# Kernel optimization log

Measured on AMD Instinct MI355X. Metric: run time of the kernel, lower is better.

Reference implementation:

```python
import jax, jax.numpy as jnp
import numpy as np

D_EMB, D_ENC, D_DEC, NH = 128, 256, 512, 8
HD = D_DEC // NH  # 64
LN_EPS = 1e-5


def lstm_scan(x_seq, h0, c0, W_ih, W_hh, b):
    # x_seq: [L, B, D_in]; PyTorch gate order i, f, g, o
    def step(carry, x_t):
        h, c = carry
        g = x_t @ W_ih.T + h @ W_hh.T + b
        i, f, gg, o = jnp.split(g, 4, axis=-1)
        c = jax.nn.sigmoid(f) * c + jax.nn.sigmoid(i) * jnp.tanh(gg)
        h = jax.nn.sigmoid(o) * jnp.tanh(c)
        return (h, c), h
    (h, c), hs = jax.lax.scan(step, (h0, c0), x_seq)
    return hs, h, c


def setup_inputs() -> dict:
    key = jax.random.key(0)
    ks = iter(jax.random.split(key, 32))
    B, L, V, NC, T = 64, 64, 32000, 2, 32
    s = 0.05
    nrm = lambda shape: jax.random.normal(next(ks), shape, jnp.float32) * s
    return dict(
        nx=jax.random.randint(next(ks), (B, L), 0, V),
        label=jax.random.randint(next(ks), (B,), 0, NC),
        start_emb=nrm((1, D_EMB)),
        tok_emb=nrm((V, D_EMB)),
        style_emb=nrm((NC, D_DEC)),
        enc_Wih_f=nrm((4 * D_ENC, D_EMB)), enc_Whh_f=nrm((4 * D_ENC, D_ENC)), enc_b_f=nrm((4 * D_ENC,)),
        enc_Wih_b=nrm((4 * D_ENC, D_EMB)), enc_Whh_b=nrm((4 * D_ENC, D_ENC)), enc_b_b=nrm((4 * D_ENC,)),
        transfer_W=nrm((D_DEC, 2 * D_ENC)),
        dec_Wih=nrm((4 * D_DEC, D_EMB)), dec_Whh=nrm((4 * D_DEC, D_DEC)), dec_b=nrm((4 * D_DEC,)),
        attn_in_w=nrm((3 * D_DEC, D_DEC)), attn_in_b=nrm((3 * D_DEC,)),
        attn_out_w=nrm((D_DEC, D_DEC)), attn_out_b=nrm((D_DEC,)),
        proj_W=nrm((V, D_DEC)), proj_b=nrm((V,)),
        ln_g=jnp.ones((D_DEC,), jnp.float32), ln_b=jnp.zeros((D_DEC,), jnp.float32),
        max_len=T,
    )


def reference(nx, label, start_emb, tok_emb, style_emb,
              enc_Wih_f, enc_Whh_f, enc_b_f, enc_Wih_b, enc_Whh_b, enc_b_b,
              transfer_W, dec_Wih, dec_Whh, dec_b,
              attn_in_w, attn_in_b, attn_out_w, attn_out_b,
              proj_W, proj_b, ln_g, ln_b, max_len):
    B, L = nx.shape
    x = tok_emb[nx]                      # [B, L, 128] (dropout = identity, eval)
    xs = jnp.transpose(x, (1, 0, 2))     # [L, B, 128]
    z = jnp.zeros((B, D_ENC), x.dtype)
    hs_f, hf, _ = lstm_scan(xs, z, z, enc_Wih_f, enc_Whh_f, enc_b_f)
    hs_b, hb, _ = lstm_scan(xs[::-1], z, z, enc_Wih_b, enc_Whh_b, enc_b_b)
    memory = jnp.concatenate([hs_f, hs_b[::-1]], axis=-1)        # [L, B, 512]
    h0 = jnp.tanh(jnp.concatenate([hf, hb], -1) @ transfer_W.T)  # [B, 512]
    c0 = style_emb[label]                                        # [B, 512]

    Wq, Wk, Wv = jnp.split(attn_in_w, 3, axis=0)
    bq, bk, bv = jnp.split(attn_in_b, 3, axis=0)
    k = (memory @ Wk.T + bk).reshape(L, B, NH, HD)
    v = (memory @ Wv.T + bv).reshape(L, B, NH, HD)
    scale = 1.0 / np.sqrt(HD).astype(np.float32)

    x0 = jnp.broadcast_to(start_emb[0], (B, D_EMB))

    def step(carry, _):
        h, c, xe = carry
        # LSTM cell (decoder, single step)
        g = xe @ dec_Wih.T + h @ dec_Whh.T + dec_b
        i, f, gg, o = jnp.split(g, 4, axis=-1)
        c = jax.nn.sigmoid(f) * c + jax.nn.sigmoid(i) * jnp.tanh(gg)
        h_ = jax.nn.sigmoid(o) * jnp.tanh(c)                     # [B, 512]
        # single-query multi-head attention against memory
        q = ((h_ @ Wq.T + bq) * scale).reshape(B, NH, HD)
        att = jax.nn.softmax(jnp.einsum('bhd,lbhd->bhl', q, k), axis=-1)
        ctx = jnp.einsum('bhl,lbhd->bhd', att, v).reshape(B, D_DEC)
        a = ctx @ attn_out_w.T + attn_out_b
        # residual + LayerNorm
        y = h_ + a
        mu = y.mean(-1, keepdims=True)
        var = ((y - mu) ** 2).mean(-1, keepdims=True)
        h = (y - mu) / jnp.sqrt(var + LN_EPS) * ln_g + ln_b
        logits_t = h @ proj_W.T + proj_b                         # [B, V]
        xe = tok_emb[jnp.argmax(logits_t, axis=-1)]              # greedy feedback
        return (h, c, xe), logits_t

    _, logits = jax.lax.scan(step, (h0, c0, x0), None, length=max_len)
    return jnp.transpose(logits, (1, 0, 2))  # [B, T, V]
```

## Files before the change

### kernel.cpp

```cpp
#include <hip/hip_runtime.h>
#include <hip/hip_bf16.h>
#include <math.h>

#define L_SEQ 64
#define B_SZ  64
#define DEMB  128
#define DENC  256
#define DDEC  512
#define NHD   8
#define HDIM  64
#define VSZ   32000
#define TDEC  32

typedef unsigned long long ull;

__device__ __forceinline__ float sigm(float x){ return 1.0f/(1.0f+expf(-x)); }
__device__ __forceinline__ int rfl(int x){ return __builtin_amdgcn_readfirstlane(x); }
__device__ __forceinline__ unsigned fmono(float f){
    unsigned u = __float_as_uint(f);
    return (u & 0x80000000u) ? ~u : (u | 0x80000000u);
}

__global__ void k_init(float* hTe, float* cTe, float* xeT, const float* start_emb){
    int i = blockIdx.x*256 + threadIdx.x;
    int stride = gridDim.x*256;
    for (int j = i; j < 2*2*DENC*B_SZ; j += stride) hTe[j] = 0.f;
    for (int j = i; j < 2*DENC*B_SZ;   j += stride) cTe[j] = 0.f;
    for (int j = i; j < DEMB*B_SZ;     j += stride) xeT[j] = start_emb[j >> 6];
}

__global__ void k_embed(const int* nx, const float* tok_emb, float* xT){
    int t = blockIdx.x;
    for (int j = threadIdx.x; j < B_SZ*DEMB; j += 256){
        int b = j >> 7; int k = j & 127;
        int row = nx[b*L_SEQ + t];
        xT[(t*DEMB + k)*B_SZ + b] = tok_emb[(size_t)row*DEMB + k];
    }
}

__global__ void k_pregates(const float* xT, const float* Wf, const float* bf,
                           const float* Wb, const float* bb, float* GpreT){
    int wid  = (blockIdx.x*256 + threadIdx.x) >> 6;
    int lane = threadIdx.x & 63;
    for (int job = wid; job < 2*L_SEQ*1024; job += 2048){
        int dir = rfl(job >> 16);
        int rem = job & 65535;
        int t   = rfl(rem >> 10);
        int row = rfl(rem & 1023);
        const float* W = dir ? Wb : Wf;
        float acc = (dir ? bb : bf)[row];
        const float4* W4 = (const float4*)(W + (size_t)row*DEMB);
        const float* xr = xT + (size_t)t*DEMB*B_SZ + lane;
        #pragma unroll 4
        for (int k4 = 0; k4 < DEMB/4; ++k4){
            float4 w = W4[k4];
            const float* hp = xr + k4*4*B_SZ;
            acc += w.x*hp[0] + w.y*hp[B_SZ] + w.z*hp[2*B_SZ] + w.w*hp[3*B_SZ];
        }
        GpreT[(size_t)job*B_SZ + lane] = acc;
    }
}

__global__ void k_enc_step(int s, const float* __restrict__ GpreT,
                           const float* __restrict__ Whh_f, const float* __restrict__ Whh_b,
                           float* hTe, float* cTe, float* memT){
    int wid  = blockIdx.x;
    int lane = threadIdx.x & 63;
    int dir = rfl(wid >> 8);
    int u   = rfl(wid & 255);
    int tpre = dir ? (63 - s) : s;
    const float* Gp = GpreT + (size_t)(dir*L_SEQ + tpre)*1024*B_SZ;
    float gi = Gp[(u      )*B_SZ + lane];
    float gf = Gp[(u + 256)*B_SZ + lane];
    float gg = Gp[(u + 512)*B_SZ + lane];
    float go = Gp[(u + 768)*B_SZ + lane];
    const float* hT  = hTe + (size_t)(s&1)*(2*DENC*B_SZ) + dir*DENC*B_SZ;
    float*       hTn = hTe + (size_t)((s+1)&1)*(2*DENC*B_SZ) + dir*DENC*B_SZ;
    const float* W = dir ? Whh_b : Whh_f;
    const float4* Wi = (const float4*)(W + (size_t)(u      )*DENC);
    const float4* Wf = (const float4*)(W + (size_t)(u + 256)*DENC);
    const float4* Wg = (const float4*)(W + (size_t)(u + 512)*DENC);
    const float4* Wo = (const float4*)(W + (size_t)(u + 768)*DENC);
    #pragma unroll 4
    for (int k4 = 0; k4 < DENC/4; ++k4){
        float4 wi = Wi[k4], wf = Wf[k4], wg = Wg[k4], wo = Wo[k4];
        const float* hp = hT + k4*4*B_SZ + lane;
        float h0 = hp[0], h1 = hp[B_SZ], h2 = hp[2*B_SZ], h3 = hp[3*B_SZ];
        gi += wi.x*h0 + wi.y*h1 + wi.z*h2 + wi.w*h3;
        gf += wf.x*h0 + wf.y*h1 + wf.z*h2 + wf.w*h3;
        gg += wg.x*h0 + wg.y*h1 + wg.z*h2 + wg.w*h3;
        go += wo.x*h0 + wo.y*h1 + wo.z*h2 + wo.w*h3;
    }
    float c  = cTe[(dir*DENC + u)*B_SZ + lane];
    float cn = sigm(gf)*c + sigm(gi)*tanhf(gg);
    float hn = sigm(go)*tanhf(cn);
    cTe[(dir*DENC + u)*B_SZ + lane] = cn;
    hTn[u*B_SZ + lane] = hn;
    int tmem = dir ? (63 - s) : s;
    memT[((size_t)tmem*DDEC + dir*DENC + u)*B_SZ + lane] = hn;
}

__global__ void k_h0(const float* hTe, const float* transfer_W, const float* style_emb,
                     const int* label, float* hTd, float* cTd){
    int u    = rfl((int)blockIdx.x);
    int lane = threadIdx.x & 63;
    const float* hf = hTe;
    const float* hb = hTe + DENC*B_SZ;
    float acc = 0.f;
    const float4* W4 = (const float4*)(transfer_W + (size_t)u*DDEC);
    #pragma unroll 4
    for (int k4 = 0; k4 < 64; ++k4){
        float4 w = W4[k4];
        const float* hp = hf + k4*4*B_SZ + lane;
        acc += w.x*hp[0] + w.y*hp[B_SZ] + w.z*hp[2*B_SZ] + w.w*hp[3*B_SZ];
    }
    #pragma unroll 4
    for (int k4 = 64; k4 < 128; ++k4){
        float4 w = W4[k4];
        const float* hp = hb + (k4-64)*4*B_SZ + lane;
        acc += w.x*hp[0] + w.y*hp[B_SZ] + w.z*hp[2*B_SZ] + w.w*hp[3*B_SZ];
    }
    hTd[u*B_SZ + lane] = tanhf(acc);
    cTd[u*B_SZ + lane] = style_emb[(size_t)label[lane]*DDEC + u];
}

__global__ void k_kv(const float* memT, const float* attn_in_w, const float* attn_in_b,
                     float* kT, float* vv){
    int wid  = (blockIdx.x*256 + threadIdx.x) >> 6;
    int lane = threadIdx.x & 63;
    for (int job = wid; job < L_SEQ*1024; job += 2048){
        int t   = rfl(job >> 10);
        int row = rfl(job & 1023);
        int wrow = 512 + row;
        const float4* W4 = (const float4*)(attn_in_w + (size_t)wrow*DDEC);
        float acc = attn_in_b[wrow];
        const float* mp = memT + (size_t)t*DDEC*B_SZ + lane;
        #pragma unroll 4
        for (int k4 = 0; k4 < 128; ++k4){
            float4 w = W4[k4];
            const float* hp = mp + k4*4*B_SZ;
            acc += w.x*hp[0] + w.y*hp[B_SZ] + w.z*hp[2*B_SZ] + w.w*hp[3*B_SZ];
        }
        if (row < 512){
            int h = row >> 6, d = row & 63;
            kT[(((size_t)lane*NHD + h)*HDIM + d)*L_SEQ + t] = acc;
        } else {
            int r2 = row - 512; int h = r2 >> 6, d = r2 & 63;
            vv[(((size_t)lane*NHD + h)*L_SEQ + t)*HDIM + d] = acc;
        }
    }
}

__global__ void k_gates(const float* __restrict__ xeT, const float* __restrict__ hTd, float* cTd,
                        const float* __restrict__ Wih, const float* __restrict__ Whh,
                        const float* __restrict__ bias, float* h_row){
    int u    = rfl((int)blockIdx.x);
    int lane = threadIdx.x & 63;
    float gi = bias[u], gf = bias[u+512], gg = bias[u+1024], go = bias[u+1536];
    {
        const float4* Wi = (const float4*)(Wih + (size_t)(u       )*DEMB);
        const float4* Wf = (const float4*)(Wih + (size_t)(u + 512 )*DEMB);
        const float4* Wg = (const float4*)(Wih + (size_t)(u + 1024)*DEMB);
        const float4* Wo = (const float4*)(Wih + (size_t)(u + 1536)*DEMB);
        #pragma unroll 4
        for (int k4 = 0; k4 < DEMB/4; ++k4){
            float4 wi = Wi[k4], wf = Wf[k4], wg = Wg[k4], wo = Wo[k4];
            const float* hp = xeT + k4*4*B_SZ + lane;
            float h0 = hp[0], h1 = hp[B_SZ], h2 = hp[2*B_SZ], h3 = hp[3*B_SZ];
            gi += wi.x*h0 + wi.y*h1 + wi.z*h2 + wi.w*h3;
            gf += wf.x*h0 + wf.y*h1 + wf.z*h2 + wf.w*h3;
            gg += wg.x*h0 + wg.y*h1 + wg.z*h2 + wg.w*h3;
            go += wo.x*h0 + wo.y*h1 + wo.z*h2 + wo.w*h3;
        }
    }
    {
        const float4* Wi = (const float4*)(Whh + (size_t)(u       )*DDEC);
        const float4* Wf = (const float4*)(Whh + (size_t)(u + 512 )*DDEC);
        const float4* Wg = (const float4*)(Whh + (size_t)(u + 1024)*DDEC);
        const float4* Wo = (const float4*)(Whh + (size_t)(u + 1536)*DDEC);
        #pragma unroll 4
        for (int k4 = 0; k4 < DDEC/4; ++k4){
            float4 wi = Wi[k4], wf = Wf[k4], wg = Wg[k4], wo = Wo[k4];
            const float* hp = hTd + k4*4*B_SZ + lane;
            float h0 = hp[0], h1 = hp[B_SZ], h2 = hp[2*B_SZ], h3 = hp[3*B_SZ];
            gi += wi.x*h0 + wi.y*h1 + wi.z*h2 + wi.w*h3;
            gf += wf.x*h0 + wf.y*h1 + wf.z*h2 + wf.w*h3;
            gg += wg.x*h0 + wg.y*h1 + wg.z*h2 + wg.w*h3;
            go += wo.x*h0 + wo.y*h1 + wo.z*h2 + wo.w*h3;
        }
    }
    float c  = cTd[u*B_SZ + lane];
    float cn = sigm(gf)*c + sigm(gi)*tanhf(gg);
    float h_ = sigm(go)*tanhf(cn);
    cTd[u*B_SZ + lane] = cn;
    h_row[(size_t)lane*DDEC + u] = h_;
}

__global__ void __launch_bounds__(256) k_attn(
        const float* __restrict__ h_row, const float* __restrict__ kT, const float* __restrict__ vv,
        const float* __restrict__ attn_in_w, const float* __restrict__ attn_in_b,
        const float* __restrict__ attn_out_w, const float* __restrict__ attn_out_b,
        const float* __restrict__ ln_g, const float* __restrict__ ln_b,
        float* hTd, float* hLN_row){
    int b = blockIdx.x, tid = threadIdx.x;
    __shared__ float hs[512], qs[512], ss[512], cx[512], ys[512];
    __shared__ float ssum[8];
    __shared__ float red[256];
    hs[tid]     = h_row[(size_t)b*512 + tid];
    hs[tid+256] = h_row[(size_t)b*512 + tid + 256];
    __syncthreads();
    for (int r = 0; r < 2; ++r){
        int row = tid + r*256;
        float acc = attn_in_b[row];
        const float4* W4 = (const float4*)(attn_in_w + (size_t)row*512);
        #pragma unroll 4
        for (int k4 = 0; k4 < 128; ++k4){
            float4 w = W4[k4];
            acc += w.x*hs[k4*4] + w.y*hs[k4*4+1] + w.z*hs[k4*4+2] + w.w*hs[k4*4+3];
        }
        qs[row] = acc * 0.125f;
    }
    __syncthreads();
    for (int r = 0; r < 2; ++r){
        int job = tid + r*256; int h = job >> 6, l = job & 63;
        const float* kp = kT + ((size_t)b*NHD + h)*HDIM*L_SEQ + l;
        float acc = 0.f;
        #pragma unroll 8
        for (int d = 0; d < 64; ++d) acc += qs[h*64 + d] * kp[d*64];
        ss[job] = acc;
    }
    __syncthreads();
    if (tid < 8){
        float m = -1e30f;
        for (int l = 0; l < 64; ++l) m = fmaxf(m, ss[tid*64 + l]);
        float s = 0.f;
        for (int l = 0; l < 64; ++l){ float e = expf(ss[tid*64 + l] - m); ss[tid*64 + l] = e; s += e; }
        ssum[tid] = s;
    }
    __syncthreads();
    for (int r = 0; r < 2; ++r){
        int job = tid + r*256; int h = job >> 6, d = job & 63;
        const float* vp = vv + ((size_t)b*NHD + h)*L_SEQ*HDIM + d;
        float acc = 0.f;
        #pragma unroll 8
        for (int l = 0; l < 64; ++l) acc += ss[h*64 + l] * vp[l*HDIM];
        cx[job] = acc / ssum[h];
    }
    __syncthreads();
    for (int r = 0; r < 2; ++r){
        int row = tid + r*256;
        float acc = attn_out_b[row];
        const float4* W4 = (const float4*)(attn_out_w + (size_t)row*512);
        #pragma unroll 4
        for (int k4 = 0; k4 < 128; ++k4){
            float4 w = W4[k4];
            acc += w.x*cx[k4*4] + w.y*cx[k4*4+1] + w.z*cx[k4*4+2] + w.w*cx[k4*4+3];
        }
        ys[row] = hs[row] + acc;
    }
    __syncthreads();
    red[tid] = ys[tid] + ys[tid+256];
    __syncthreads();
    for (int off = 128; off > 0; off >>= 1){ if (tid < off) red[tid] += red[tid+off]; __syncthreads(); }
    float mu = red[0] * (1.f/512.f);
    __syncthreads();
    float d0 = ys[tid] - mu, d1 = ys[tid+256] - mu;
    red[tid] = d0*d0 + d1*d1;
    __syncthreads();
    for (int off = 128; off > 0; off >>= 1){ if (tid < off) red[tid] += red[tid+off]; __syncthreads(); }
    float rstd = 1.f / sqrtf(red[0]*(1.f/512.f) + 1e-5f);
    for (int r = 0; r < 2; ++r){
        int i = tid + r*256;
        float hv = (ys[i] - mu) * rstd * ln_g[i] + ln_b[i];
        hLN_row[(size_t)b*512 + i] = hv;
        hTd[(size_t)i*64 + b] = hv;
    }
}

__global__ void __launch_bounds__(256) k_proj(int t, const float* __restrict__ hTd,
                       const float* __restrict__ proj_W, const float* __restrict__ proj_b,
                       float* __restrict__ out, ull* __restrict__ partials){
    int wid  = (blockIdx.x*256 + threadIdx.x) >> 6;
    int lane = threadIdx.x & 63;
    int n0 = rfl(wid << 4);
    float acc[16];
    #pragma unroll
    for (int j = 0; j < 16; ++j) acc[j] = proj_b[n0 + j];
    const float* W = proj_W + (size_t)n0*DDEC;
    #pragma unroll 2
    for (int k4 = 0; k4 < 128; ++k4){
        float h0 = hTd[(k4*4+0)*B_SZ + lane];
        float h1 = hTd[(k4*4+1)*B_SZ + lane];
        float h2 = hTd[(k4*4+2)*B_SZ + lane];
        float h3 = hTd[(k4*4+3)*B_SZ + lane];
        #pragma unroll
        for (int j = 0; j < 16; ++j){
            float4 w = *(const float4*)(W + (size_t)j*DDEC + k4*4);
            acc[j] += w.x*h0 + w.y*h1 + w.z*h2 + w.w*h3;
        }
    }
    ull m = 0;
    float* op = out + (size_t)lane*(TDEC*VSZ) + (size_t)t*VSZ + n0;
    #pragma unroll
    for (int j = 0; j < 16; ++j){
        op[j] = acc[j];
        ull p = ((ull)fmono(acc[j]) << 32) | (unsigned)(~(unsigned)(n0 + j));
        m = (p > m) ? p : m;
    }
    partials[(size_t)lane*2048 + wid] = m;
}

__global__ void k_fin(const ull* __restrict__ partials, const float* __restrict__ tok_emb, float* xeT){
    int b = blockIdx.x, tid = threadIdx.x;
    __shared__ ull red[128];
    __shared__ int sidx;
    ull m = 0;
    for (int j = tid; j < 2000; j += 128){
        ull p = partials[(size_t)b*2048 + j];
        if (p > m) m = p;
    }
    red[tid] = m; __syncthreads();
    for (int off = 64; off > 0; off >>= 1){
        if (tid < off){ if (red[tid+off] > red[tid]) red[tid] = red[tid+off]; }
        __syncthreads();
    }
    if (tid == 0) sidx = (int)(~(unsigned)(red[0] & 0xffffffffull));
    __syncthreads();
    int idx = sidx;
    xeT[tid*B_SZ + b] = tok_emb[(size_t)idx*DEMB + tid];
}

extern "C" void kernel_launch(void* const* d_in, const int* in_sizes, int n_in,
                              void* d_out, int out_size, void* d_ws, size_t ws_size,
                              hipStream_t stream){
    (void)in_sizes; (void)n_in; (void)out_size; (void)ws_size;
    const int*   nx        = (const int*)d_in[0];
    const int*   label     = (const int*)d_in[1];
    const float* start_emb = (const float*)d_in[2];
    const float* tok_emb   = (const float*)d_in[3];
    const float* style_emb = (const float*)d_in[4];
    const float* enc_Wih_f = (const float*)d_in[5];
    const float* enc_Whh_f = (const float*)d_in[6];
    const float* enc_b_f   = (const float*)d_in[7];
    const float* enc_Wih_b = (const float*)d_in[8];
    const float* enc_Whh_b = (const float*)d_in[9];
    const float* enc_b_b   = (const float*)d_in[10];
    const float* transfer_W= (const float*)d_in[11];
    const float* dec_Wih   = (const float*)d_in[12];
    const float* dec_Whh   = (const float*)d_in[13];
    const float* dec_b     = (const float*)d_in[14];
    const float* attn_in_w = (const float*)d_in[15];
    const float* attn_in_b = (const float*)d_in[16];
    const float* attn_out_w= (const float*)d_in[17];
    const float* attn_out_b= (const float*)d_in[18];
    const float* proj_W    = (const float*)d_in[19];
    const float* proj_b    = (const float*)d_in[20];
    const float* ln_g      = (const float*)d_in[21];
    const float* ln_b      = (const float*)d_in[22];
    float* out = (float*)d_out;
    float* ws  = (float*)d_ws;

    size_t off = 0;
    float* xT    = ws + off; off += (size_t)L_SEQ*DEMB*B_SZ;
    float* GpreT = ws + off; off += (size_t)2*L_SEQ*1024*B_SZ;
    float* memT  = ws + off; off += (size_t)L_SEQ*DDEC*B_SZ;
    float* kT    = ws + off; off += (size_t)B_SZ*NHD*HDIM*L_SEQ;
    float* vv    = ws + off; off += (size_t)B_SZ*NHD*L_SEQ*HDIM;
    float* hTe   = ws + off; off += 2*2*DENC*B_SZ;
    float* cTe   = ws + off; off += 2*DENC*B_SZ;
    float* hTd   = ws + off; off += DDEC*B_SZ;
    float* cTd   = ws + off; off += DDEC*B_SZ;
    float* h_row = ws + off; off += B_SZ*DDEC;
    float* hLN   = ws + off; off += B_SZ*DDEC;
    float* xeT   = ws + off; off += DEMB*B_SZ;
    ull* partials = (ull*)(ws + off); off += (size_t)B_SZ*2048*2;

    k_init<<<64, 256, 0, stream>>>(hTe, cTe, xeT, start_emb);
    k_embed<<<64, 256, 0, stream>>>(nx, tok_emb, xT);
    k_pregates<<<512, 256, 0, stream>>>(xT, enc_Wih_f, enc_b_f, enc_Wih_b, enc_b_b, GpreT);
    for (int s = 0; s < 64; ++s)
        k_enc_step<<<512, 64, 0, stream>>>(s, GpreT, enc_Whh_f, enc_Whh_b, hTe, cTe, memT);
    k_h0<<<512, 64, 0, stream>>>(hTe, transfer_W, style_emb, label, hTd, cTd);
    k_kv<<<512, 256, 0, stream>>>(memT, attn_in_w, attn_in_b, kT, vv);
    for (int t = 0; t < 32; ++t){
        k_gates<<<512, 64, 0, stream>>>(xeT, hTd, cTd, dec_Wih, dec_Whh, dec_b, h_row);
        k_attn<<<64, 256, 0, stream>>>(h_row, kT, vv, attn_in_w, attn_in_b,
                                       attn_out_w, attn_out_b, ln_g, ln_b, hTd, hLN);
        k_proj<<<500, 256, 0, stream>>>(t, hTd, proj_W, proj_b, out, partials);
        k_fin<<<64, 128, 0, stream>>>(partials, tok_emb, xeT);
    }
}
```

Before: 9.384 ms.

## Register-block pregates and K/V projections; reduce argmax partials per block

The encoder input-gate and attention K/V projection kernels now have each wavefront compute 16 output rows at once. Each activation load is reused across those 16 rows instead of being reloaded per row, with __restrict__ and launch bounds added. The projection kernel writes logits with float4 stores and does a block-level shared-memory max before writing partials. This cuts partials per batch row from 2000 to 500, so the final argmax kernel reads less. The cost is higher register pressure and fewer parallel jobs in the pregate and K/V kernels.

```diff
diff --git a/kernel.cpp b/kernel.cpp
--- a/kernel.cpp
+++ b/kernel.cpp
@@ -38,26 +38,34 @@
     }
 }
 
-__global__ void k_pregates(const float* xT, const float* Wf, const float* bf,
-                           const float* Wb, const float* bb, float* GpreT){
+__global__ void __launch_bounds__(256) k_pregates(
+        const float* __restrict__ xT, const float* __restrict__ Wf, const float* __restrict__ bf,
+        const float* __restrict__ Wb, const float* __restrict__ bb, float* __restrict__ GpreT){
     int wid  = (blockIdx.x*256 + threadIdx.x) >> 6;
     int lane = threadIdx.x & 63;
-    for (int job = wid; job < 2*L_SEQ*1024; job += 2048){
-        int dir = rfl(job >> 16);
-        int rem = job & 65535;
-        int t   = rfl(rem >> 10);
-        int row = rfl(rem & 1023);
-        const float* W = dir ? Wb : Wf;
-        float acc = (dir ? bb : bf)[row];
-        const float4* W4 = (const float4*)(W + (size_t)row*DEMB);
+    for (int job = wid; job < 2*L_SEQ*64; job += 2048){
+        int dir = rfl(job >> 12);
+        int rem = job & 4095;
+        int t   = rfl(rem >> 6);
+        int n0  = rfl((rem & 63) << 4);
+        const float* W = (dir ? Wb : Wf) + (size_t)n0*DEMB;
+        const float* bias = dir ? bb : bf;
+        float acc[16];
+        #pragma unroll
+        for (int j = 0; j < 16; ++j) acc[j] = bias[n0 + j];
         const float* xr = xT + (size_t)t*DEMB*B_SZ + lane;
-        #pragma unroll 4
         for (int k4 = 0; k4 < DEMB/4; ++k4){
-            float4 w = W4[k4];
-            const float* hp = xr + k4*4*B_SZ;
-            acc += w.x*hp[0] + w.y*hp[B_SZ] + w.z*hp[2*B_SZ] + w.w*hp[3*B_SZ];
-        }
-        GpreT[(size_t)job*B_SZ + lane] = acc;
+            float h0 = xr[(k4*4+0)*B_SZ], h1 = xr[(k4*4+1)*B_SZ];
+            float h2 = xr[(k4*4+2)*B_SZ], h3 = xr[(k4*4+3)*B_SZ];
+            #pragma unroll
+            for (int j = 0; j < 16; ++j){
+                float4 w = *(const float4*)(W + (size_t)j*DEMB + k4*4);
+                acc[j] += w.x*h0 + w.y*h1 + w.z*h2 + w.w*h3;
+            }
+        }
+        float* gp = GpreT + ((size_t)(dir*L_SEQ + t)*1024 + n0)*B_SZ + lane;
+        #pragma unroll
+        for (int j = 0; j < 16; ++j) gp[j*B_SZ] = acc[j];
     }
 }
 
@@ -124,29 +132,42 @@
     cTd[u*B_SZ + lane] = style_emb[(size_t)label[lane]*DDEC + u];
 }
 
-__global__ void k_kv(const float* memT, const float* attn_in_w, const float* attn_in_b,
-                     float* kT, float* vv){
+__global__ void __launch_bounds__(256) k_kv(
+        const float* __restrict__ memT, const float* __restrict__ attn_in_w,
+        const float* __restrict__ attn_in_b, float* __restrict__ kT, float* __restrict__ vv){
     int wid  = (blockIdx.x*256 + threadIdx.x) >> 6;
     int lane = threadIdx.x & 63;
-    for (int job = wid; job < L_SEQ*1024; job += 2048){
-        int t   = rfl(job >> 10);
-        int row = rfl(job & 1023);
-        int wrow = 512 + row;
-        const float4* W4 = (const float4*)(attn_in_w + (size_t)wrow*DDEC);
-        float acc = attn_in_b[wrow];
+    for (int job = wid; job < L_SEQ*64; job += 2048){
+        int t  = rfl(job >> 6);
+        int n0 = rfl((job & 63) << 4);
+        int wrow0 = 512 + n0;
+        const float* W = attn_in_w + (size_t)wrow0*DDEC;
+        float acc[16];
+        #pragma unroll
+        for (int j = 0; j < 16; ++j) acc[j] = attn_in_b[wrow0 + j];
         const float* mp = memT + (size_t)t*DDEC*B_SZ + lane;
-        #pragma unroll 4
-        for (int k4 = 0; k4 < 128; ++k4){
-            float4 w = W4[k4];
-            const float* hp = mp + k4*4*B_SZ;
-            acc += w.x*hp[0] + w.y*hp[B_SZ] + w.z*hp[2*B_SZ] + w.w*hp[3*B_SZ];
-        }
-        if (row < 512){
-            int h = row >> 6, d = row & 63;
-            kT[(((size_t)lane*NHD + h)*HDIM + d)*L_SEQ + t] = acc;
+        for (int k4 = 0; k4 < DDEC/4; ++k4){
+            float h0 = mp[(k4*4+0)*B_SZ], h1 = mp[(k4*4+1)*B_SZ];
+            float h2 = mp[(k4*4+2)*B_SZ], h3 = mp[(k4*4+3)*B_SZ];
+            #pragma unroll
+            for (int j = 0; j < 16; ++j){
+                float4 w = *(const float4*)(W + (size_t)j*DDEC + k4*4);
+                acc[j] += w.x*h0 + w.y*h1 + w.z*h2 + w.w*h3;
+            }
+        }
+        if (n0 < 512){
+            int h = n0 >> 6, d0 = n0 & 63;
+            float* kp = kT + (((size_t)lane*NHD + h)*HDIM + d0)*L_SEQ + t;
+            #pragma unroll
+            for (int j = 0; j < 16; ++j) kp[j*L_SEQ] = acc[j];
         } else {
-            int r2 = row - 512; int h = r2 >> 6, d = r2 & 63;
-            vv[(((size_t)lane*NHD + h)*L_SEQ + t)*HDIM + d] = acc;
+            int r2 = n0 - 512; int h = r2 >> 6, d0 = r2 & 63;
+            float* vp = vv + (((size_t)lane*NHD + h)*L_SEQ + t)*HDIM + d0;
+            #pragma unroll
+            for (int j4 = 0; j4 < 4; ++j4){
+                float4 o; o.x = acc[j4*4]; o.y = acc[j4*4+1]; o.z = acc[j4*4+2]; o.w = acc[j4*4+3];
+                *(float4*)(vp + j4*4) = o;
+            }
         }
     }
 }
@@ -282,6 +303,7 @@
                        float* __restrict__ out, ull* __restrict__ partials){
     int wid  = (blockIdx.x*256 + threadIdx.x) >> 6;
     int lane = threadIdx.x & 63;
+    int wv   = threadIdx.x >> 6;
     int n0 = rfl(wid << 4);
     float acc[16];
     #pragma unroll
@@ -302,12 +324,23 @@
     ull m = 0;
     float* op = out + (size_t)lane*(TDEC*VSZ) + (size_t)t*VSZ + n0;
     #pragma unroll
-    for (int j = 0; j < 16; ++j){
-        op[j] = acc[j];
-        ull p = ((ull)fmono(acc[j]) << 32) | (unsigned)(~(unsigned)(n0 + j));
-        m = (p > m) ? p : m;
-    }
-    partials[(size_t)lane*2048 + wid] = m;
+    for (int j4 = 0; j4 < 4; ++j4){
+        float4 o; o.x = acc[j4*4]; o.y = acc[j4*4+1]; o.z = acc[j4*4+2]; o.w = acc[j4*4+3];
+        *(float4*)(op + j4*4) = o;
+        #pragma unroll
+        for (int j = j4*4; j < j4*4+4; ++j){
+            ull p = ((ull)fmono(acc[j]) << 32) | (unsigned)(~(unsigned)(n0 + j));
+            m = (p > m) ? p : m;
+        }
+    }
+    __shared__ ull red[4][64];
+    red[wv][lane] = m;
+    __syncthreads();
+    if (wv == 0){
+        ull a = red[0][lane], b2 = red[1][lane], c = red[2][lane], d = red[3][lane];
+        if (b2 > a) a = b2; if (c > a) a = c; if (d > a) a = d;
+        partials[(size_t)lane*512 + blockIdx.x] = a;
+    }
 }
 
 __global__ void k_fin(const ull* __restrict__ partials, const float* __restrict__ tok_emb, float* xeT){
@@ -315,8 +348,8 @@
     __shared__ ull red[128];
     __shared__ int sidx;
     ull m = 0;
-    for (int j = tid; j < 2000; j += 128){
-        ull p = partials[(size_t)b*2048 + j];
+    for (int j = tid; j < 500; j += 128){
+        ull p = partials[(size_t)b*512 + j];
         if (p > m) m = p;
     }
     red[tid] = m; __syncthreads();
@@ -373,7 +406,7 @@
     float* h_row = ws + off; off += B_SZ*DDEC;
     float* hLN   = ws + off; off += B_SZ*DDEC;
     float* xeT   = ws + off; off += DEMB*B_SZ;
-    ull* partials = (ull*)(ws + off); off += (size_t)B_SZ*2048*2;
+    ull* partials = (ull*)(ws + off); off += (size_t)B_SZ*512*2;
 
     k_init<<<64, 256, 0, stream>>>(hTe, cTe, xeT, start_emb);
     k_embed<<<64, 256, 0, stream>>>(nx, tok_emb, xT);
```

After: 8.529 ms. 9.1% less time.
